# Performance work log

Measured on AMD Instinct MI355X. Metric: run time of the kernel, lower is better.

Reference implementation:

```python
import jax, jax.numpy as jnp
import numpy as np

B, T, U, D = 2, 256, 64, 512
INNER, VOCAB = 512, 4096


def setup_inputs() -> dict:
    key = jax.random.key(0)
    k1, k2, k3, k4, k5, k6 = jax.random.split(key, 6)
    s1 = 1.0 / np.sqrt(2 * D)      # torch Linear init scale for fan_in=2D
    s2 = 1.0 / np.sqrt(INNER)
    return {
        "enc_state": jax.random.normal(k1, (B, T, D), dtype=jnp.float32),
        "dec_state": jax.random.normal(k2, (B, U, D), dtype=jnp.float32),
        "W1": jax.random.normal(k3, (INNER, 2 * D), dtype=jnp.float32) * s1,
        "b1": jax.random.normal(k4, (INNER,), dtype=jnp.float32) * s1,
        "W2": jax.random.normal(k5, (VOCAB, INNER), dtype=jnp.float32) * s2,
        "b2": jax.random.normal(k6, (VOCAB,), dtype=jnp.float32) * s2,
    }


def reference(enc_state, dec_state, W1, b1, W2, b2):
    # JointNet: repeat enc (B,T,1,D)->(B,T,U,D), dec (B,1,U,D)->(B,T,U,D),
    # concat -> Linear(2D,inner) -> tanh -> Linear(inner,vocab).
    # Equivalent efficient form: split W1 into enc/dec halves, project each
    # sequence once, broadcast-add (the concat+Linear decomposes exactly).
    d = enc_state.shape[-1]
    We, Wd = W1[:, :d], W1[:, d:]
    enc_proj = jnp.einsum("btd,id->bti", enc_state, We)   # (B,T,inner)
    dec_proj = jnp.einsum("bud,id->bui", dec_state, Wd)   # (B,U,inner)
    h = jnp.tanh(enc_proj[:, :, None, :] + dec_proj[:, None, :, :] + b1)  # (B,T,U,inner)
    logits = jnp.einsum("btui,vi->btuv", h, W2) + b2       # (B,T,U,vocab)
    return logits
```

## Files before the change

### kernel.cpp

```cpp
#include <hip/hip_runtime.h>
#include <hip/hip_bf16.h>
#include <stdint.h>

#define T_DIM 256
#define U_DIM 64
#define D_DIM 512
#define NIN 512
#define NV 4096

typedef __bf16 bf16x8 __attribute__((ext_vector_type(8)));
typedef float f32x4 __attribute__((ext_vector_type(4)));

static __device__ __forceinline__ unsigned short f2bf(float x) {
  union { float f; unsigned int u; } v; v.f = x;
  unsigned int r = v.u + 0x7FFFu + ((v.u >> 16) & 1u);
  return (unsigned short)(r >> 16);
}

static __device__ __forceinline__ void gload_lds16(const unsigned short* g, void* l) {
  __builtin_amdgcn_global_load_lds(
      (__attribute__((address_space(1))) void*)(unsigned short*)g,
      (__attribute__((address_space(3))) void*)l, 16, 0, 0);
}

__global__ __launch_bounds__(256) void prep_kernel(const float* __restrict__ W2,
                                                   unsigned short* __restrict__ W2b,
                                                   const float* __restrict__ enc,
                                                   const float* __restrict__ dec,
                                                   const float* __restrict__ W1,
                                                   float* __restrict__ ep0,
                                                   float* __restrict__ ep1,
                                                   float* __restrict__ dp0,
                                                   float* __restrict__ dp1) {
  __shared__ unsigned short As[128 * 32];
  __shared__ unsigned short Bs[128 * 32];
  const int tid = threadIdx.x;

  if (blockIdx.x < 1024) {
    int q = blockIdx.x * 256 + tid;
    const float4 v0 = *(const float4*)(W2 + (size_t)q * 8);
    const float4 v1 = *(const float4*)(W2 + (size_t)q * 8 + 4);
    union { unsigned short s[8]; uint4 u; } o;
    o.s[0] = f2bf(v0.x); o.s[1] = f2bf(v0.y); o.s[2] = f2bf(v0.z); o.s[3] = f2bf(v0.w);
    o.s[4] = f2bf(v1.x); o.s[5] = f2bf(v1.y); o.s[6] = f2bf(v1.z); o.s[7] = f2bf(v1.w);
    *(uint4*)(W2b + (size_t)q * 8) = o.u;
    return;
  }

  const int pbid = blockIdx.x - 1024;
  const int tile_m = pbid >> 3;
  const int kh = (pbid >> 2) & 1;
  const int tile_n = pbid & 3;
  const bool is_dec = (tile_m == 4);
  const float* X = is_dec ? dec : enc;
  const int xrow0 = is_dec ? 0 : tile_m * 128;
  const int wcol0 = is_dec ? D_DIM : 0;
  float* outp = is_dec ? (kh ? dp1 : dp0) : (kh ? ep1 : ep0);

  const int lane = tid & 63;
  const int wv = tid >> 6;
  const int wr = wv >> 1, wc = wv & 1;
  const int arow = tid >> 1;
  const int acol = (tid & 1) * 16;

  f32x4 acc[4][4] = {};

  const float* pa = X + (size_t)(xrow0 + arow) * D_DIM + acol;
  const float* pb = W1 + (size_t)(tile_n * 128 + arow) * (2 * D_DIM) + wcol0 + acol;

  for (int k0 = kh * 256; k0 < kh * 256 + 256; k0 += 32) {
    float4 av0 = *(const float4*)(pa + k0);
    float4 av1 = *(const float4*)(pa + k0 + 4);
    float4 av2 = *(const float4*)(pa + k0 + 8);
    float4 av3 = *(const float4*)(pa + k0 + 12);
    float4 bv0 = *(const float4*)(pb + k0);
    float4 bv1 = *(const float4*)(pb + k0 + 4);
    float4 bv2 = *(const float4*)(pb + k0 + 8);
    float4 bv3 = *(const float4*)(pb + k0 + 12);
    __syncthreads();
    union { unsigned short s[8]; uint4 u; } u0, u1, w0, w1;
    u0.s[0] = f2bf(av0.x); u0.s[1] = f2bf(av0.y); u0.s[2] = f2bf(av0.z); u0.s[3] = f2bf(av0.w);
    u0.s[4] = f2bf(av1.x); u0.s[5] = f2bf(av1.y); u0.s[6] = f2bf(av1.z); u0.s[7] = f2bf(av1.w);
    u1.s[0] = f2bf(av2.x); u1.s[1] = f2bf(av2.y); u1.s[2] = f2bf(av2.z); u1.s[3] = f2bf(av2.w);
    u1.s[4] = f2bf(av3.x); u1.s[5] = f2bf(av3.y); u1.s[6] = f2bf(av3.z); u1.s[7] = f2bf(av3.w);
    w0.s[0] = f2bf(bv0.x); w0.s[1] = f2bf(bv0.y); w0.s[2] = f2bf(bv0.z); w0.s[3] = f2bf(bv0.w);
    w0.s[4] = f2bf(bv1.x); w0.s[5] = f2bf(bv1.y); w0.s[6] = f2bf(bv1.z); w0.s[7] = f2bf(bv1.w);
    w1.s[0] = f2bf(bv2.x); w1.s[1] = f2bf(bv2.y); w1.s[2] = f2bf(bv2.z); w1.s[3] = f2bf(bv2.w);
    w1.s[4] = f2bf(bv3.x); w1.s[5] = f2bf(bv3.y); w1.s[6] = f2bf(bv3.z); w1.s[7] = f2bf(bv3.w);
    *(uint4*)&As[arow * 32 + acol] = u0.u;
    *(uint4*)&As[arow * 32 + acol + 8] = u1.u;
    *(uint4*)&Bs[arow * 32 + acol] = w0.u;
    *(uint4*)&Bs[arow * 32 + acol + 8] = w1.u;
    __syncthreads();
    bf16x8 af[4], bff[4];
#pragma unroll
    for (int mi = 0; mi < 4; ++mi)
      af[mi] = *(const bf16x8*)&As[(wr * 64 + mi * 16 + (lane & 15)) * 32 + (lane >> 4) * 8];
#pragma unroll
    for (int ni = 0; ni < 4; ++ni)
      bff[ni] = *(const bf16x8*)&Bs[(wc * 64 + ni * 16 + (lane & 15)) * 32 + (lane >> 4) * 8];
#pragma unroll
    for (int mi = 0; mi < 4; ++mi)
#pragma unroll
      for (int ni = 0; ni < 4; ++ni)
        acc[mi][ni] = __builtin_amdgcn_mfma_f32_16x16x32_bf16(af[mi], bff[ni], acc[mi][ni], 0, 0, 0);
  }

#pragma unroll
  for (int mi = 0; mi < 4; ++mi) {
#pragma unroll
    for (int r = 0; r < 4; ++r) {
      int row = xrow0 + wr * 64 + mi * 16 + ((lane >> 4) << 2) + r;
      float* po = outp + (size_t)row * NIN + tile_n * 128 + wc * 64 + (lane & 15);
#pragma unroll
      for (int ni = 0; ni < 4; ++ni) po[ni * 16] = acc[mi][ni][r];
    }
  }
}

__global__ __launch_bounds__(256) void h_kernel(const float* __restrict__ ep0,
                                                const float* __restrict__ ep1,
                                                const float* __restrict__ dp0,
                                                const float* __restrict__ dp1,
                                                const float* __restrict__ b1,
                                                unsigned short* __restrict__ Hb) {
  int q = blockIdx.x * 256 + threadIdx.x;
  int m = q >> 6;
  int i0 = (q & 63) << 3;
  size_t eoff = (size_t)(m >> 6) * NIN + i0;
  size_t doff = (size_t)((m >> 14) * U_DIM + (m & 63)) * NIN + i0;
  float4 e0 = *(const float4*)(ep0 + eoff);
  float4 e1 = *(const float4*)(ep0 + eoff + 4);
  float4 f0 = *(const float4*)(ep1 + eoff);
  float4 f1 = *(const float4*)(ep1 + eoff + 4);
  float4 d0 = *(const float4*)(dp0 + doff);
  float4 d1 = *(const float4*)(dp0 + doff + 4);
  float4 g0 = *(const float4*)(dp1 + doff);
  float4 g1 = *(const float4*)(dp1 + doff + 4);
  float4 c0 = *(const float4*)(b1 + i0);
  float4 c1 = *(const float4*)(b1 + i0 + 4);
  float x[8] = { e0.x + f0.x + d0.x + g0.x + c0.x, e0.y + f0.y + d0.y + g0.y + c0.y,
                 e0.z + f0.z + d0.z + g0.z + c0.z, e0.w + f0.w + d0.w + g0.w + c0.w,
                 e1.x + f1.x + d1.x + g1.x + c1.x, e1.y + f1.y + d1.y + g1.y + c1.y,
                 e1.z + f1.z + d1.z + g1.z + c1.z, e1.w + f1.w + d1.w + g1.w + c1.w };
  union { unsigned short s[8]; uint4 u; } o;
#pragma unroll
  for (int j = 0; j < 8; ++j) {
    float ex = __expf(2.0f * x[j]);
    float t = 1.0f - 2.0f / (ex + 1.0f);
    o.s[j] = f2bf(t);
  }
  *(uint4*)(Hb + (size_t)q * 8) = o.u;
}

__global__ __launch_bounds__(256, 2) void gemm_kernel(const unsigned short* __restrict__ Hb,
                                                      const unsigned short* __restrict__ W2b,
                                                      const float* __restrict__ b2,
                                                      float* __restrict__ out) {
  __shared__ __align__(16) char smem[73728];
  const int tid = threadIdx.x;
  const int lane = tid & 63;
  const int wv = tid >> 6;
  const int wr = wv >> 1, wc = wv & 1;
  const int bid = blockIdx.x;

  const int xcd = bid & 7;
  const int idx = bid >> 3;
  const int sup = idx >> 5;
  const int within = idx & 31;
  const int tm = (xcd << 4) | ((sup >> 2) << 2) | (within >> 3);
  const int tn = ((sup & 3) << 3) | (within & 7);
  const int m0 = tm * 256, n0 = tn * 128;

  const int srow = tid >> 2;
  const int segp = ((((tid & 3) - ((tid >> 3) & 3)) & 3) << 3);
  const unsigned short* pA = Hb + (size_t)(m0 + srow) * 512 + segp;
  const unsigned short* pB = W2b + (size_t)(n0 + srow) * 512 + segp;
  const int dstOff = tid << 4;
  const int laneA = ((lane & 15) << 6) | ((((lane >> 4) + ((lane >> 1) & 7)) & 3) << 4);

  f32x4 acc[8][4] = {};
  bf16x8 af[8], bf_[4];

#define STAGE(T, BUF) do { \
    gload_lds16(pA + (size_t)(T) * 32,                smem + (BUF) * 24576 + dstOff); \
    gload_lds16(pA + (size_t)(T) * 32 + 64 * 512,     smem + (BUF) * 24576 + 4096 + dstOff); \
    gload_lds16(pA + (size_t)(T) * 32 + 128 * 512,    smem + (BUF) * 24576 + 8192 + dstOff); \
    gload_lds16(pA + (size_t)(T) * 32 + 192 * 512,    smem + (BUF) * 24576 + 12288 + dstOff); \
    gload_lds16(pB + (size_t)(T) * 32,                smem + (BUF) * 24576 + 16384 + dstOff); \
    gload_lds16(pB + (size_t)(T) * 32 + 64 * 512,     smem + (BUF) * 24576 + 20480 + dstOff); \
  } while (0)
#define BAR() __builtin_amdgcn_s_barrier()
#define SCHED0() __builtin_amdgcn_sched_barrier(0)
#define VMCNT(N) asm volatile("s_waitcnt vmcnt(" #N ")" ::: "memory")

  STAGE(0, 0);
  STAGE(1, 1);

#pragma unroll
  for (int k = 0; k < 16; ++k) {
    const int cur = k % 3;
    if (k < 14) { STAGE(k + 2, (k + 2) % 3); }
    if (k < 14) { VMCNT(12); } else if (k == 14) { VMCNT(6); } else { VMCNT(0); }
    BAR();
    SCHED0();
#pragma unroll
    for (int mi = 0; mi < 8; ++mi)
      af[mi] = *(const bf16x8*)(smem + cur * 24576 + ((wr * 8 + mi) << 10) + laneA);
#pragma unroll
    for (int ni = 0; ni < 4; ++ni)
      bf_[ni] = *(const bf16x8*)(smem + cur * 24576 + 16384 + ((wc * 4 + ni) << 10) + laneA);
    __builtin_amdgcn_s_setprio(1);
#pragma unroll
    for (int mi = 0; mi < 8; ++mi)
#pragma unroll
      for (int ni = 0; ni < 4; ++ni)
        acc[mi][ni] = __builtin_amdgcn_mfma_f32_16x16x32_bf16(af[mi], bf_[ni], acc[mi][ni], 0, 0, 0);
    __builtin_amdgcn_s_setprio(0);
    SCHED0();
    BAR();
  }

#undef STAGE
#undef BAR
#undef SCHED0
#undef VMCNT

  float b2v[4];
#pragma unroll
  for (int ni = 0; ni < 4; ++ni) b2v[ni] = b2[n0 + wc * 64 + ni * 16 + (lane & 15)];
#pragma unroll
  for (int mi = 0; mi < 8; ++mi) {
#pragma unroll
    for (int r = 0; r < 4; ++r) {
      int row = m0 + wr * 128 + mi * 16 + ((lane >> 4) << 2) + r;
      float* po = out + (size_t)row * NV + n0 + wc * 64 + (lane & 15);
#pragma unroll
      for (int ni = 0; ni < 4; ++ni)
        __builtin_nontemporal_store(acc[mi][ni][r] + b2v[ni], po + ni * 16);
    }
  }
}

extern "C" void kernel_launch(void* const* d_in, const int* in_sizes, int n_in,
                              void* d_out, int out_size, void* d_ws, size_t ws_size,
                              hipStream_t stream) {
  const float* enc = (const float*)d_in[0];
  const float* dec = (const float*)d_in[1];
  const float* W1  = (const float*)d_in[2];
  const float* b1  = (const float*)d_in[3];
  const float* W2  = (const float*)d_in[4];
  const float* b2  = (const float*)d_in[5];
  float* out = (float*)d_out;

  char* ws = (char*)d_ws;
  unsigned short* W2b = (unsigned short*)(ws);
  float* ep0 = (float*)(ws + 4194304);
  float* ep1 = (float*)(ws + 5242880);
  float* dp0 = (float*)(ws + 6291456);
  float* dp1 = (float*)(ws + 6553600);
  unsigned short* Hb = (unsigned short*)(ws + 6815744);

  hipLaunchKernelGGL(prep_kernel, dim3(1064), dim3(256), 0, stream,
                     W2, W2b, enc, dec, W1, ep0, ep1, dp0, dp1);
  hipLaunchKernelGGL(h_kernel, dim3(8192), dim3(256), 0, stream, ep0, ep1, dp0, dp1, b1, Hb);
  hipLaunchKernelGGL(gemm_kernel, dim3(4096), dim3(256), 0, stream, Hb, W2b, b2, out);
}
```

Before: 200.8 us.

## Load W2 operand directly into registers and use one barrier per k-step

```diff
diff --git a/kernel.cpp b/kernel.cpp
--- a/kernel.cpp
+++ b/kernel.cpp
@@ -157,7 +157,7 @@
                                                       const unsigned short* __restrict__ W2b,
                                                       const float* __restrict__ b2,
                                                       float* __restrict__ out) {
-  __shared__ __align__(16) char smem[73728];
+  __shared__ __align__(16) char smem[49152];
   const int tid = threadIdx.x;
   const int lane = tid & 63;
   const int wv = tid >> 6;
@@ -175,60 +175,78 @@
   const int srow = tid >> 2;
   const int segp = ((((tid & 3) - ((tid >> 3) & 3)) & 3) << 3);
   const unsigned short* pA = Hb + (size_t)(m0 + srow) * 512 + segp;
-  const unsigned short* pB = W2b + (size_t)(n0 + srow) * 512 + segp;
   const int dstOff = tid << 4;
   const int laneA = ((lane & 15) << 6) | ((((lane >> 4) + ((lane >> 1) & 7)) & 3) << 4);
 
+  const unsigned short* pBd = W2b + (size_t)(n0 + wc * 64 + (lane & 15)) * 512 + ((lane >> 4) << 3);
+
   f32x4 acc[8][4] = {};
-  bf16x8 af[8], bf_[4];
+  bf16x8 af[8], bqA[4], bqB[4];
+
+  float b2v[4];
+#pragma unroll
+  for (int ni = 0; ni < 4; ++ni) b2v[ni] = b2[n0 + wc * 64 + ni * 16 + (lane & 15)];
 
 #define STAGE(T, BUF) do { \
-    gload_lds16(pA + (size_t)(T) * 32,                smem + (BUF) * 24576 + dstOff); \
-    gload_lds16(pA + (size_t)(T) * 32 + 64 * 512,     smem + (BUF) * 24576 + 4096 + dstOff); \
-    gload_lds16(pA + (size_t)(T) * 32 + 128 * 512,    smem + (BUF) * 24576 + 8192 + dstOff); \
-    gload_lds16(pA + (size_t)(T) * 32 + 192 * 512,    smem + (BUF) * 24576 + 12288 + dstOff); \
-    gload_lds16(pB + (size_t)(T) * 32,                smem + (BUF) * 24576 + 16384 + dstOff); \
-    gload_lds16(pB + (size_t)(T) * 32 + 64 * 512,     smem + (BUF) * 24576 + 20480 + dstOff); \
+    gload_lds16(pA + (size_t)(T) * 32,             smem + (BUF) * 16384 + dstOff); \
+    gload_lds16(pA + (size_t)(T) * 32 + 64 * 512,  smem + (BUF) * 16384 + 4096 + dstOff); \
+    gload_lds16(pA + (size_t)(T) * 32 + 128 * 512, smem + (BUF) * 16384 + 8192 + dstOff); \
+    gload_lds16(pA + (size_t)(T) * 32 + 192 * 512, smem + (BUF) * 16384 + 12288 + dstOff); \
   } while (0)
 #define BAR() __builtin_amdgcn_s_barrier()
 #define SCHED0() __builtin_amdgcn_sched_barrier(0)
-#define VMCNT(N) asm volatile("s_waitcnt vmcnt(" #N ")" ::: "memory")
-
+#define VMCNT_(N) asm volatile("s_waitcnt vmcnt(" #N ")" ::: "memory")
+#define VMCNT(N) VMCNT_(N)
+
+#define LOADB(DST, K) do { \
+    _Pragma("unroll") for (int ni = 0; ni < 4; ++ni) \
+      DST[ni] = *(const bf16x8*)(pBd + (size_t)ni * 16 * 512 + (K) * 32); \
+  } while (0)
+
+#define ITER(K, W, CURB, NXTB) do { \
+    VMCNT(W); \
+    BAR(); \
+    SCHED0(); \
+    if ((K) < 15) { LOADB(NXTB, (K) + 1); } \
+    if ((K) < 14) { STAGE((K) + 2, ((K) + 2) % 3); } \
+    _Pragma("unroll") for (int mi = 0; mi < 8; ++mi) \
+      af[mi] = *(const bf16x8*)(smem + ((K) % 3) * 16384 + ((wr * 8 + mi) << 10) + laneA); \
+    __builtin_amdgcn_s_setprio(1); \
+    _Pragma("unroll") for (int mi = 0; mi < 8; ++mi) \
+      _Pragma("unroll") for (int ni = 0; ni < 4; ++ni) \
+        acc[mi][ni] = __builtin_amdgcn_mfma_f32_16x16x32_bf16(af[mi], CURB[ni], acc[mi][ni], 0, 0, 0); \
+    __builtin_amdgcn_s_setprio(0); \
+  } while (0)
+
+  LOADB(bqA, 0);
   STAGE(0, 0);
   STAGE(1, 1);
 
-#pragma unroll
-  for (int k = 0; k < 16; ++k) {
-    const int cur = k % 3;
-    if (k < 14) { STAGE(k + 2, (k + 2) % 3); }
-    if (k < 14) { VMCNT(12); } else if (k == 14) { VMCNT(6); } else { VMCNT(0); }
-    BAR();
-    SCHED0();
-#pragma unroll
-    for (int mi = 0; mi < 8; ++mi)
-      af[mi] = *(const bf16x8*)(smem + cur * 24576 + ((wr * 8 + mi) << 10) + laneA);
-#pragma unroll
-    for (int ni = 0; ni < 4; ++ni)
-      bf_[ni] = *(const bf16x8*)(smem + cur * 24576 + 16384 + ((wc * 4 + ni) << 10) + laneA);
-    __builtin_amdgcn_s_setprio(1);
-#pragma unroll
-    for (int mi = 0; mi < 8; ++mi)
-#pragma unroll
-      for (int ni = 0; ni < 4; ++ni)
-        acc[mi][ni] = __builtin_amdgcn_mfma_f32_16x16x32_bf16(af[mi], bf_[ni], acc[mi][ni], 0, 0, 0);
-    __builtin_amdgcn_s_setprio(0);
-    SCHED0();
-    BAR();
-  }
+  ITER(0, 4, bqA, bqB);
+  ITER(1, 8, bqB, bqA);
+  ITER(2, 8, bqA, bqB);
+  ITER(3, 8, bqB, bqA);
+  ITER(4, 8, bqA, bqB);
+  ITER(5, 8, bqB, bqA);
+  ITER(6, 8, bqA, bqB);
+  ITER(7, 8, bqB, bqA);
+  ITER(8, 8, bqA, bqB);
+  ITER(9, 8, bqB, bqA);
+  ITER(10, 8, bqA, bqB);
+  ITER(11, 8, bqB, bqA);
+  ITER(12, 8, bqA, bqB);
+  ITER(13, 8, bqB, bqA);
+  ITER(14, 8, bqA, bqB);
+  ITER(15, 4, bqB, bqA);
 
 #undef STAGE
 #undef BAR
 #undef SCHED0
+#undef VMCNT_
 #undef VMCNT
-
-  float b2v[4];
-#pragma unroll
-  for (int ni = 0; ni < 4; ++ni) b2v[ni] = b2[n0 + wc * 64 + ni * 16 + (lane & 15)];
+#undef LOADB
+#undef ITER
+
 #pragma unroll
   for (int mi = 0; mi < 8; ++mi) {
 #pragma unroll
```

Result: slower. 249.5 us (+24.3%).
